# Kernel optimization log

Measured on AMD Instinct MI355X. Metric: run time of the kernel, lower is better.

Reference implementation:

```python
import jax, jax.numpy as jnp
import numpy as np

B, N, H, DQK, DV = 2, 2048, 16, 128, 128
E = H * DV
CHUNK = 64


def setup_inputs() -> dict:
    key = jax.random.key(0)
    ks = jax.random.split(key, 11)
    w = lambda k: jax.random.normal(k, (E, E), jnp.float32) * 0.02
    return {
        "x": jax.random.normal(ks[0], (B, N, E), jnp.float32),
        "prev_state": jnp.zeros((B, H, DQK, DV), jnp.float32),
        "Wq": w(ks[1]), "bq": jnp.zeros((E,), jnp.float32),
        "Wk": w(ks[2]), "bk": jnp.zeros((E,), jnp.float32),
        "Wv": w(ks[3]), "bv": jnp.zeros((E,), jnp.float32),
        "Wg": w(ks[4]), "bg": jnp.zeros((E,), jnp.float32),
        "Wo": w(ks[5]), "bo": jnp.zeros((E,), jnp.float32),
        "start_idx": 0,
    }


def _mul_i(t):
    # multiply interleaved complex pairs by i: (a, b) -> (-b, a)
    t2 = t.reshape(*t.shape[:-1], -1, 2)
    return jnp.stack((-t2[..., 1], t2[..., 0]), axis=-1).reshape(t.shape)


def reference(x, prev_state, Wq, bq, Wk, bk, Wv, bv, Wg, bg, Wo, bo, start_idx):
    b, n, e = x.shape
    h, dqk, dv, c = H, DQK, DV, CHUNK
    q = (x @ Wq.T + bq).reshape(b, n, h, dqk)
    k = (x @ Wk.T + bk).reshape(b, n, h, dqk)
    v = (x @ Wv.T + bv).reshape(b, n, h, dv)

    # xPos-style theta shift (rotary on interleaved pairs), applied along the sequence dim
    lin = jnp.linspace(0.0, 1.0, dqk // 2)
    thetas = jnp.repeat(1.0 / (10000.0 ** lin), 2).astype(x.dtype)  # (dqk,)
    idx = (start_idx + jnp.arange(n)).astype(x.dtype)
    ang = idx[:, None] * thetas[None, :]  # (n, dqk)
    sin = jnp.sin(ang)[None, :, None, :]
    cos = jnp.cos(ang)[None, :, None, :]
    q = q * cos + _mul_i(q) * sin
    k = k * cos + _mul_i(k) * sin
    k = k / jnp.sqrt(jnp.asarray(dqk, x.dtype))

    # per-head decays: 1 - 2^(-5 - h)
    gamma = 1.0 - jnp.exp2(-5.0 - jnp.arange(h, dtype=x.dtype))  # (h,)
    i = jnp.arange(c, dtype=x.dtype)
    mask = i[:, None] >= i[None, :]
    Dmat = jnp.where(mask, gamma[:, None, None] ** jnp.where(mask, i[:, None] - i[None, :], 0.0), 0.0)  # (h,c,c)
    cross_decay = gamma[:, None] ** (i[None, :] + 1.0)   # (h,c)
    kv_decay = gamma[:, None] ** (c - 1.0 - i[None, :])  # (h,c)
    chunk_decay = gamma ** c                              # (h,)

    nc = n // c
    qc = q.reshape(b, nc, c, h, dqk).transpose(1, 0, 3, 2, 4)  # (nc,b,h,c,dqk)
    kc = k.reshape(b, nc, c, h, dqk).transpose(1, 0, 3, 2, 4)
    vc = v.reshape(b, nc, c, h, dv).transpose(1, 0, 3, 2, 4)

    def step(S, qkv):
        qi, ki, vi = qkv  # (b,h,c,d)
        att = jnp.einsum('bhid,bhjd->bhij', qi, ki) * Dmat[None]
        o = jnp.einsum('bhij,bhje->bhie', att, vi)
        o = o + jnp.einsum('bhid,bhde->bhie', qi, S) * cross_decay[None, :, :, None]
        S_new = S * chunk_decay[None, :, None, None] + jnp.einsum('bhjd,bhje->bhde', ki * kv_decay[None, :, :, None], vi)
        return S_new, o

    state, outs = jax.lax.scan(step, prev_state, (qc, kc, vc))
    ret = outs.transpose(1, 0, 3, 2, 4).reshape(b, n, h, dv)

    # GroupNorm(num_groups=h, affine=False): normalize each head over dv
    mu = ret.mean(-1, keepdims=True)
    var = ((ret - mu) ** 2).mean(-1, keepdims=True)
    ret = ((ret - mu) / jnp.sqrt(var + 1e-6)).reshape(b, n, e)

    gate = jax.nn.silu(x @ Wg.T + bg)
    out = (ret * gate) @ Wo.T + bo
    return out, state
```

## Files before the change

kernel.cpp:

```cpp
#include <hip/hip_runtime.h>
#include <hip/hip_bf16.h>
#include <stdint.h>

#define B_   2
#define N_   2048
#define H_   16
#define DQK_ 128
#define DV_  128
#define E_   2048
#define CH_  64
#define NC_  32
#define M_   (B_*N_)
#define QKVG_LD 8192

using bf16x8 = __attribute__((ext_vector_type(8))) __bf16;
using f32x4  = __attribute__((ext_vector_type(4))) float;
typedef __hip_bfloat16 bf16_t;

__device__ __forceinline__ void gload_lds16(const void* g, void* l) {
  __builtin_amdgcn_global_load_lds(
      (const __attribute__((address_space(1))) void*)(uintptr_t)g,
      (__attribute__((address_space(3))) void*)(uint32_t)(uintptr_t)l,
      16, 0, 0);
}

__device__ __forceinline__ float head_log2g(int h) {
  return (float)(log2(1.0 - exp2((double)(-5 - h))));
}

__device__ __forceinline__ float bfu2f(unsigned short u) {
  unsigned int t = (unsigned int)u << 16; float f;
  __builtin_memcpy(&f, &t, 4); return f;
}
__device__ __forceinline__ unsigned short f2bfu(float f) {
  bf16_t b = __float2bfloat16(f);
  unsigned short u; __builtin_memcpy(&u, &b, 2); return u;
}

__global__ __launch_bounds__(256)
void cvt_all_kernel(const float* __restrict__ x,
                    const float* __restrict__ Wq, const float* __restrict__ Wk,
                    const float* __restrict__ Wv, const float* __restrict__ Wg,
                    const float* __restrict__ Wo,
                    const float* __restrict__ bq, const float* __restrict__ bk,
                    const float* __restrict__ bv, const float* __restrict__ bg,
                    bf16_t* __restrict__ xb, bf16_t* __restrict__ wcat,
                    bf16_t* __restrict__ wob, float* __restrict__ bcat) {
  const int NX = 2097152, NW = 1048576;
  int g = blockIdx.x * 256 + threadIdx.x;
  const float* s; bf16_t* d; int si, di;
  if (g < NX) { s = x; si = g; d = xb; di = g; }
  else if (g < NX + 4*NW) {
    int t = g - NX; int r = t / NW; si = t - r*NW;
    s = (r==0) ? Wq : (r==1) ? Wk : (r==2) ? Wv : Wg; d = wcat; di = t;
  } else if (g < NX + 5*NW) {
    si = g - NX - 4*NW; s = Wo; d = wob; di = si;
  } else {
    int j = g - (NX + 5*NW);
    int which = j >> 9, i = j & 511;
    const float* bs = (which==0) ? bq : (which==1) ? bk : (which==2) ? bv : bg;
    ((float4*)bcat)[which*512 + i] = ((const float4*)bs)[i];
    return;
  }
  float4 v = ((const float4*)s)[si];
  ushort4 p;
  p.x = f2bfu(v.x); p.y = f2bfu(v.y); p.z = f2bfu(v.z); p.w = f2bfu(v.w);
  ((ushort4*)d)[di] = p;
}

template<bool OUT_BF16, int NSUB>
__global__ __launch_bounds__(512, 2)
void gemm8_kernel(const bf16_t* __restrict__ A, const bf16_t* __restrict__ Bw,
                  const float* __restrict__ bias, void* __restrict__ Cout,
                  int K, int ldc, int tilesM) {
  extern __shared__ char smem[];
  const int nwg = gridDim.x;
  const int bid = blockIdx.x;
  const int cpx = nwg >> 3;
  const int swz = (bid & 7) * cpx + (bid >> 3);
  const int tm = swz % tilesM, tn = swz / tilesM;
  const int rowT0 = tm * 256, colT0 = tn * (64 * NSUB);
  const int tid = threadIdx.x, wave = tid >> 6, lane = tid & 63;
  const int wr = wave >> 2, wc = wave & 3;
  const int l16 = lane & 15, lhi = lane >> 4;
  const int NKT = K >> 6;

  const int sw = ((tid & 7) * 16) ^ (((tid >> 3) & 7) << 4);
  const size_t aOff = (size_t)(rowT0 + (tid >> 3)) * K + (sw >> 1);
  const size_t bOff = (size_t)(colT0 + (tid >> 3)) * K + (sw >> 1);
  const uint32_t wl = wave * 1024;

  auto stage = [&](int h) {
    const int ktp = h >> 2, r = h & 3, buf = ktp & 1;
    const int k0 = ktp << 6;
    if (r < 2) {
      const uint32_t base = 65536u + buf * (8192u*NSUB) + r * (4096u*NSUB) + wl;
#pragma unroll
      for (int L = 0; L < NSUB/2; L++)
        gload_lds16(Bw + bOff + (size_t)(r * (NSUB*32) + L * 64) * K + k0,
                    smem + base + L * 8192);
    } else {
      const int half = r - 2;
      const uint32_t base = buf * 32768u + half * 16384u + wl;
#pragma unroll
      for (int L = 0; L < 2; L++)
        gload_lds16(A + aOff + (size_t)(half * 128 + L * 64) * K + k0,
                    smem + base + L * 8192);
    }
  };

  for (int h = 0; h < 6; h++) stage(h);
  if constexpr (NSUB == 4) asm volatile("s_waitcnt vmcnt(4)" ::: "memory");
  else                     asm volatile("s_waitcnt vmcnt(2)" ::: "memory");
  __builtin_amdgcn_s_barrier();
  asm volatile("" ::: "memory");
  __builtin_amdgcn_sched_barrier(0);

  f32x4 acc[8][NSUB] = {};
  bf16x8 bfr[NSUB][2], bnx[2][2];

#pragma unroll
  for (int n = 0; n < 2; n++) {
    const int r = wc * (16*NSUB) + n * 16 + l16;
#pragma unroll
    for (int ks = 0; ks < 2; ks++) {
      const int cb = ks * 64 + lhi * 16;
      bnx[n][ks] = *(const bf16x8*)(smem + 65536u + r * 128 + (cb ^ ((r & 7) << 4)));
    }
  }

  for (int kt = 0; kt < NKT; kt++) {
    const int cur = kt & 1;
    const uint32_t aB = cur * 32768u;
    const uint32_t bB = 65536u + cur * (8192u*NSUB);
#pragma unroll
    for (int p = 0; p < 4; p++) {
      if (p == 0) {
#pragma unroll
        for (int n = 0; n < 2; n++)
#pragma unroll
          for (int ks = 0; ks < 2; ks++) bfr[n][ks] = bnx[n][ks];
        if constexpr (NSUB == 4) {
#pragma unroll
          for (int n = 2; n < 4; n++) {
            const int r = wc * (16*NSUB) + n * 16 + l16;
#pragma unroll
            for (int ks = 0; ks < 2; ks++) {
              const int cb = ks * 64 + lhi * 16;
              bfr[n][ks] = *(const bf16x8*)(smem + bB + r * 128 + (cb ^ ((r & 7) << 4)));
            }
          }
        }
      }
      bf16x8 afr[2][2];
#pragma unroll
      for (int mm = 0; mm < 2; mm++) {
        const int r = wr * 128 + p * 32 + mm * 16 + l16;
#pragma unroll
        for (int ks = 0; ks < 2; ks++) {
          const int cb = ks * 64 + lhi * 16;
          afr[mm][ks] = *(const bf16x8*)(smem + aB + r * 128 + (cb ^ ((r & 7) << 4)));
        }
      }
      const int h = 4 * kt + p + 6;
      if (h < 4 * NKT) stage(h);
      __builtin_amdgcn_s_barrier();
      asm volatile("s_waitcnt lgkmcnt(0)" ::: "memory");
      __builtin_amdgcn_sched_barrier(0);
      __builtin_amdgcn_s_setprio(1);
#pragma unroll
      for (int mm = 0; mm < 2; mm++)
#pragma unroll
        for (int n = 0; n < NSUB; n++)
#pragma unroll
          for (int ks = 0; ks < 2; ks++)
            acc[2 * p + mm][n] = __builtin_amdgcn_mfma_f32_16x16x32_bf16(
                afr[mm][ks], bfr[n][ks], acc[2 * p + mm][n], 0, 0, 0);
      __builtin_amdgcn_s_setprio(0);
      if (p == 2) {
        if constexpr (NSUB == 4) asm volatile("s_waitcnt vmcnt(6)" ::: "memory");
        else                     asm volatile("s_waitcnt vmcnt(5)" ::: "memory");
      }
      if (p == 3) {
        if (kt < NKT - 2) {
          if constexpr (NSUB == 4) asm volatile("s_waitcnt vmcnt(4)" ::: "memory");
          else                     asm volatile("s_waitcnt vmcnt(2)" ::: "memory");
        } else if (kt == NKT - 2) {
          asm volatile("s_waitcnt vmcnt(0)" ::: "memory");
        }
        if (kt + 1 < NKT) {
          const uint32_t bN = 65536u + ((kt + 1) & 1) * (8192u*NSUB);
#pragma unroll
          for (int n = 0; n < 2; n++) {
            const int r = wc * (16*NSUB) + n * 16 + l16;
#pragma unroll
            for (int ks = 0; ks < 2; ks++) {
              const int cb = ks * 64 + lhi * 16;
              bnx[n][ks] = *(const bf16x8*)(smem + bN + r * 128 + (cb ^ ((r & 7) << 4)));
            }
          }
        }
      }
      __builtin_amdgcn_s_barrier();
      asm volatile("" ::: "memory");
      __builtin_amdgcn_sched_barrier(0);
    }
  }

#pragma unroll
  for (int m = 0; m < 8; m++) {
    const int rbase = rowT0 + wr * 128 + m * 16 + lhi * 4;
#pragma unroll
    for (int n = 0; n < NSUB; n++) {
      const int col = colT0 + wc * (16*NSUB) + n * 16 + l16;
      const float bv = bias[col];
#pragma unroll
      for (int j = 0; j < 4; j++) {
        float v = acc[m][n][j] + bv;
        if (OUT_BF16) ((bf16_t*)Cout)[(size_t)(rbase + j) * ldc + col] = __float2bfloat16(v);
        else          ((float*)Cout)[(size_t)(rbase + j) * ldc + col] = v;
      }
    }
  }
}

__global__ void rotary_kernel(bf16_t* __restrict__ q, bf16_t* __restrict__ k,
                              const int* __restrict__ startp) {
  int t = blockIdx.x * 256 + threadIdx.x;
  if (t >= B_*N_*H_*16) return;
  int dg = t & 15;
  int rest = t >> 4;
  int n = (rest >> 4) & (N_ - 1);
  int h = rest & 15;
  float pos = (float)(startp[0] + n);
  size_t base = (size_t)(rest >> 4) * QKVG_LD + h * 128 + dg * 8;
  bf16x8 qv = *(const bf16x8*)(q + base);
  bf16x8 kv = *(const bf16x8*)(k + base);
  bf16x8 qo, ko;
  const float KS = 0.08838834764831843f;
#pragma unroll
  for (int p = 0; p < 4; p++) {
    int j = dg * 4 + p;
    float theta = exp2f(-13.287712379549449f * ((float)j * (1.0f/63.0f)));
    float ang = pos * theta;
    float s, c;
    sincosf(ang, &s, &c);
    float qa = (float)qv[2*p], qb = (float)qv[2*p+1];
    float ka = (float)kv[2*p], kb = (float)kv[2*p+1];
    qo[2*p]   = (__bf16)(qa*c - qb*s);
    qo[2*p+1] = (__bf16)(qb*c + qa*s);
    ko[2*p]   = (__bf16)((ka*c - kb*s) * KS);
    ko[2*p+1] = (__bf16)((kb*c + ka*s) * KS);
  }
  *(bf16x8*)(q + base) = qo;
  *(bf16x8*)(k + base) = ko;
}

__global__ __launch_bounds__(256)
void chunk_kvt_kernel(const bf16_t* __restrict__ kb, const bf16_t* __restrict__ vb,
                      bf16_t* __restrict__ kvt) {
  __shared__ alignas(16) char lds[32768];
  char* vts = lds;
  char* kts = lds + 16384;

  const int tid = threadIdx.x, wave = tid >> 6, lane = tid & 63;
  const int l16 = lane & 15, lhi = lane >> 4;
  const int blk = blockIdx.x;
  const int bh = blk >> 5, ch = blk & 31;
  const int h = bh & (H_ - 1);
  const float log2g = head_log2g(h);
  const int n0 = ch * 64;

  const size_t bhbase = (size_t)(bh >> 4) * N_ * QKVG_LD + (size_t)h * 128;

#pragma unroll
  for (int it = 0; it < 4; it++) {
    int j = it*16 + (tid >> 4);
    int e0 = (tid & 15) * 8;
    bf16x8 vv = *(const bf16x8*)(vb + bhbase + (size_t)(n0 + j)*QKVG_LD + e0);
    bf16x8 kk = *(const bf16x8*)(kb + bhbase + (size_t)(n0 + j)*QKVG_LD + e0);
    float kvd = exp2f((float)(63 - j) * log2g);
#pragma unroll
    for (int m = 0; m < 8; m++) {
      int e = e0 + m;
      *(__bf16*)(vts + e*128 + ((j*2) ^ ((e&7)<<4))) = vv[m];
      *(__bf16*)(kts + e*128 + ((j*2) ^ ((e&7)<<4))) = (__bf16)((float)kk[m] * kvd);
    }
  }
  __syncthreads();

  f32x4 acc[2][8] = {};
#pragma unroll
  for (int kk2 = 0; kk2 < 2; kk2++) {
#pragma unroll
    for (int et = 0; et < 2; et++) {
      int e = (2*wave + et)*16 + l16;
      bf16x8 vf = *(const bf16x8*)(vts + e*128 + (((kk2*32 + lhi*8)*2) ^ ((e&7)<<4)));
#pragma unroll
      for (int dt = 0; dt < 8; dt++) {
        int d = dt*16 + l16;
        bf16x8 kf = *(const bf16x8*)(kts + d*128 + (((kk2*32 + lhi*8)*2) ^ ((d&7)<<4)));
        acc[et][dt] = __builtin_amdgcn_mfma_f32_16x16x32_bf16(vf, kf, acc[et][dt], 0, 0, 0);
      }
    }
  }

  const size_t obase = (size_t)blk * 16384;
#pragma unroll
  for (int et = 0; et < 2; et++)
#pragma unroll
    for (int dt = 0; dt < 8; dt++)
#pragma unroll
      for (int j = 0; j < 4; j++) {
        int e = (2*wave + et)*16 + lhi*4 + j;
        int d = dt*16 + l16;
        kvt[obase + e*128 + d] = __float2bfloat16(acc[et][dt][j]);
      }
}

__global__ __launch_bounds__(256)
void state_scan_kernel(const bf16_t* __restrict__ kvt, const float* __restrict__ prev,
                       bf16_t* __restrict__ sbft, float* __restrict__ out_state) {
  int p = blockIdx.x * 256 + threadIdx.x;
  int bh = p >> 14;
  int ed = p & 16383;
  int e = ed >> 7, d = ed & 127;
  int h = bh & (H_ - 1);
  const float cdecay = exp2f(64.0f * head_log2g(h));

  float S = prev[(size_t)bh*16384 + d*128 + e];
  size_t boff = (size_t)bh * (NC_*16384) + ed;
  for (int ch = 0; ch < NC_; ch++) {
    sbft[boff] = __float2bfloat16(S);
    S = S * cdecay + __bfloat162float(kvt[boff]);
    boff += 16384;
  }
  out_state[(size_t)bh*16384 + d*128 + e] = S;
}

__global__ __launch_bounds__(256)
void chunk_out_kernel(const bf16_t* __restrict__ qb, const bf16_t* __restrict__ kb,
                      const bf16_t* __restrict__ vb, const bf16_t* __restrict__ gb,
                      const bf16_t* __restrict__ sbft, bf16_t* __restrict__ gated) {
  __shared__ alignas(16) char lds[32768];
  char* vts = lds;
  char* ats = lds + 16384;
  float* o_lds = (float*)lds;

  const int tid = threadIdx.x, wave = tid >> 6, lane = tid & 63;
  const int l16 = lane & 15, lhi = lane >> 4;
  const int blk = blockIdx.x;
  const int bh = blk >> 5, ch = blk & 31;
  const int h = bh & (H_ - 1);
  const int b = bh >> 4;
  const float log2g = head_log2g(h);
  const int n0 = ch * 64;

  const size_t bhbase = (size_t)b * N_ * QKVG_LD + (size_t)h * 128;
  const bf16_t* Srow = sbft + (size_t)blk * 16384;

#pragma unroll
  for (int it = 0; it < 4; it++) {
    int j = it*16 + (tid >> 4);
    int e0 = (tid & 15) * 8;
    bf16x8 vv = *(const bf16x8*)(vb + bhbase + (size_t)(n0 + j)*QKVG_LD + e0);
#pragma unroll
    for (int m = 0; m < 8; m++) {
      int e = e0 + m;
      *(__bf16*)(vts + e*128 + ((j*2) ^ ((e&7)<<4))) = vv[m];
    }
  }

  bf16x8 qf[4];
#pragma unroll
  for (int dk = 0; dk < 4; dk++)
    qf[dk] = *(const bf16x8*)(qb + bhbase + (size_t)(n0 + wave*16 + l16)*QKVG_LD + dk*32 + lhi*8);

  f32x4 aacc[4] = {};
#pragma unroll
  for (int jt = 0; jt < 4; jt++) {
#pragma unroll
    for (int dk = 0; dk < 4; dk++) {
      bf16x8 kf = *(const bf16x8*)(kb + bhbase + (size_t)(n0 + jt*16 + l16)*QKVG_LD + dk*32 + lhi*8);
      aacc[jt] = __builtin_amdgcn_mfma_f32_16x16x32_bf16(qf[dk], kf, aacc[jt], 0, 0, 0);
    }
  }
#pragma unroll
  for (int jt = 0; jt < 4; jt++)
#pragma unroll
    for (int j = 0; j < 4; j++) {
      int i = wave*16 + lhi*4 + j;
      int jc = jt*16 + l16;
      aacc[jt][j] *= (i >= jc) ? exp2f((float)(i - jc) * log2g) : 0.0f;
    }

#pragma unroll
  for (int jt = 0; jt < 4; jt++)
#pragma unroll
    for (int j = 0; j < 4; j++) {
      int i = wave*16 + lhi*4 + j;
      int jc = jt*16 + l16;
      *(__bf16*)(ats + i*128 + ((jc*2) ^ ((i&7)<<4))) = (__bf16)aacc[jt][j];
    }
  __syncthreads();

  f32x4 oacc[8] = {};
#pragma unroll
  for (int et = 0; et < 8; et++) {
#pragma unroll
    for (int dk = 0; dk < 4; dk++) {
      int e = et*16 + l16;
      bf16x8 sf = *(const bf16x8*)(Srow + e*128 + dk*32 + lhi*8);
      oacc[et] = __builtin_amdgcn_mfma_f32_16x16x32_bf16(qf[dk], sf, oacc[et], 0, 0, 0);
    }
  }
#pragma unroll
  for (int j = 0; j < 4; j++) {
    int i = wave*16 + lhi*4 + j;
    float f = exp2f((float)(i + 1) * log2g);
#pragma unroll
    for (int et = 0; et < 8; et++) oacc[et][j] *= f;
  }

#pragma unroll
  for (int kk2 = 0; kk2 < 2; kk2++) {
    int i = wave*16 + l16;
    bf16x8 af = *(const bf16x8*)(ats + i*128 + (((kk2*32 + lhi*8)*2) ^ ((i&7)<<4)));
#pragma unroll
    for (int et = 0; et < 8; et++) {
      int e = et*16 + l16;
      bf16x8 vf = *(const bf16x8*)(vts + e*128 + (((kk2*32 + lhi*8)*2) ^ ((e&7)<<4)));
      oacc[et] = __builtin_amdgcn_mfma_f32_16x16x32_bf16(af, vf, oacc[et], 0, 0, 0);
    }
  }

  __syncthreads();
#pragma unroll
  for (int et = 0; et < 8; et++)
#pragma unroll
    for (int j = 0; j < 4; j++) {
      int i = wave*16 + lhi*4 + j;
      o_lds[i*128 + et*16 + l16] = oacc[et][j];
    }
  __syncthreads();

  for (int rr = 0; rr < 16; rr++) {
    int r = wave*16 + rr;
    float2 xv = *(const float2*)&o_lds[r*128 + lane*2];
    float s = xv.x + xv.y, ss = xv.x*xv.x + xv.y*xv.y;
#pragma unroll
    for (int off = 1; off < 64; off <<= 1) {
      s  += __shfl_xor(s, off);
      ss += __shfl_xor(ss, off);
    }
    float mu  = s * (1.0f/128.0f);
    float inv = rsqrtf(ss * (1.0f/128.0f) - mu*mu + 1e-6f);
    size_t grow = (size_t)b * N_ + (n0 + r);
    unsigned int gg = *(const unsigned int*)(gb + grow*QKVG_LD + h*128 + lane*2);
    float g0 = bfu2f((unsigned short)(gg & 0xffff));
    float g1 = bfu2f((unsigned short)(gg >> 16));
    float r0 = (xv.x - mu) * inv * (g0 / (1.0f + expf(-g0)));
    float r1 = (xv.y - mu) * inv * (g1 / (1.0f + expf(-g1)));
    ushort2 o2; o2.x = f2bfu(r0); o2.y = f2bfu(r1);
    *(ushort2*)(gated + grow*2048 + h*128 + lane*2) = o2;
  }
}

extern "C" void kernel_launch(void* const* d_in, const int* in_sizes, int n_in,
                              void* d_out, int out_size, void* d_ws, size_t ws_size,
                              hipStream_t stream) {
  const float* x    = (const float*)d_in[0];
  const float* prev = (const float*)d_in[1];
  const float* Wq = (const float*)d_in[2];  const float* bq = (const float*)d_in[3];
  const float* Wk = (const float*)d_in[4];  const float* bk = (const float*)d_in[5];
  const float* Wv = (const float*)d_in[6];  const float* bv = (const float*)d_in[7];
  const float* Wg = (const float*)d_in[8];  const float* bg = (const float*)d_in[9];
  const float* Wo = (const float*)d_in[10]; const float* bo = (const float*)d_in[11];
  const int* startp = (const int*)d_in[12];

  float* out = (float*)d_out;
  float* out_state = out + (size_t)B_*N_*E_;

  char* w = (char*)d_ws;
  const size_t XN = (size_t)B_*N_*E_;
  const size_t WN = (size_t)E_*E_;
  bf16_t* xb   = (bf16_t*)w;             w += XN*2;
  bf16_t* qkvg = (bf16_t*)w;             w += (size_t)M_*QKVG_LD*2;
  bf16_t* wob  = (bf16_t*)w;             w += WN*2;
  char*   wcat_region = w;               w += 4*WN*2;
  bf16_t* wcat = (bf16_t*)wcat_region;
  bf16_t* sbft = (bf16_t*)w;             w += (size_t)B_*H_*NC_*16384*2;
  bf16_t* kvt   = (bf16_t*)wcat_region;
  float*  bcat  = (float*)sbft;

  hipFuncSetAttribute(reinterpret_cast<const void*>(gemm8_kernel<true,4>),
                      hipFuncAttributeMaxDynamicSharedMemorySize, 131072);
  hipFuncSetAttribute(reinterpret_cast<const void*>(gemm8_kernel<false,2>),
                      hipFuncAttributeMaxDynamicSharedMemorySize, 98304);

  cvt_all_kernel<<<28680, 256, 0, stream>>>(x, Wq, Wk, Wv, Wg, Wo, bq, bk, bv, bg,
                                            xb, wcat, wob, bcat);

  gemm8_kernel<true,4><<<512, 512, 131072, stream>>>(xb, wcat, bcat, (void*)qkvg,
                                                     E_, QKVG_LD, 16);

  rotary_kernel<<<(B_*N_*H_*16)/256, 256, 0, stream>>>(qkvg, qkvg + 2048, startp);

  chunk_kvt_kernel<<<B_*H_*NC_, 256, 0, stream>>>(qkvg + 2048, qkvg + 4096, kvt);
  state_scan_kernel<<<(B_*H_*16384)/256, 256, 0, stream>>>(kvt, prev, sbft, out_state);
  chunk_out_kernel<<<B_*H_*NC_, 256, 0, stream>>>(qkvg, qkvg + 2048, qkvg + 4096,
                                                  qkvg + 6144, sbft, xb );

  gemm8_kernel<false,2><<<256, 512, 98304, stream>>>(xb, wob, bo, (void*)out,
                                                     E_, E_, 16);
}
```

Before: 286.4 us.

## Fuse rotary embedding into chunk kernels and remap GEMM tile ordering

Result: slower. 306.7 us (+7.1%).

```diff
diff --git a/kernel.cpp b/kernel.cpp
--- a/kernel.cpp
+++ b/kernel.cpp
@@ -17,6 +17,9 @@
 using f32x4  = __attribute__((ext_vector_type(4))) float;
 typedef __hip_bfloat16 bf16_t;
 
+#define ROT_C 0.21091607f
+#define KS_   0.08838834764831843f
+
 __device__ __forceinline__ void gload_lds16(const void* g, void* l) {
   __builtin_amdgcn_global_load_lds(
       (const __attribute__((address_space(1))) void*)(uintptr_t)g,
@@ -35,6 +38,19 @@
 __device__ __forceinline__ unsigned short f2bfu(float f) {
   bf16_t b = __float2bfloat16(f);
   unsigned short u; __builtin_memcpy(&u, &b, 2); return u;
+}
+
+__device__ __forceinline__ void rot8(const bf16x8& v, float pos, int jp0,
+                                     float scale, float* out) {
+#pragma unroll
+  for (int p = 0; p < 4; p++) {
+    float theta = exp2f(-ROT_C * (float)(jp0 + p));
+    float ang = pos * theta, s, c;
+    sincosf(ang, &s, &c);
+    float a = (float)v[2*p], b = (float)v[2*p+1];
+    out[2*p]   = (a*c - b*s) * scale;
+    out[2*p+1] = (b*c + a*s) * scale;
+  }
 }
 
 __global__ __launch_bounds__(256)
@@ -72,13 +88,13 @@
 __global__ __launch_bounds__(512, 2)
 void gemm8_kernel(const bf16_t* __restrict__ A, const bf16_t* __restrict__ Bw,
                   const float* __restrict__ bias, void* __restrict__ Cout,
-                  int K, int ldc, int tilesM) {
+                  int K, int ldc, int tilesN) {
   extern __shared__ char smem[];
   const int nwg = gridDim.x;
   const int bid = blockIdx.x;
   const int cpx = nwg >> 3;
   const int swz = (bid & 7) * cpx + (bid >> 3);
-  const int tm = swz % tilesM, tn = swz / tilesM;
+  const int tn = swz % tilesN, tm = swz / tilesN;
   const int rowT0 = tm * 256, colT0 = tn * (64 * NSUB);
   const int tid = threadIdx.x, wave = tid >> 6, lane = tid & 63;
   const int wr = wave >> 2, wc = wave & 3;
@@ -224,41 +240,9 @@
   }
 }
 
-__global__ void rotary_kernel(bf16_t* __restrict__ q, bf16_t* __restrict__ k,
-                              const int* __restrict__ startp) {
-  int t = blockIdx.x * 256 + threadIdx.x;
-  if (t >= B_*N_*H_*16) return;
-  int dg = t & 15;
-  int rest = t >> 4;
-  int n = (rest >> 4) & (N_ - 1);
-  int h = rest & 15;
-  float pos = (float)(startp[0] + n);
-  size_t base = (size_t)(rest >> 4) * QKVG_LD + h * 128 + dg * 8;
-  bf16x8 qv = *(const bf16x8*)(q + base);
-  bf16x8 kv = *(const bf16x8*)(k + base);
-  bf16x8 qo, ko;
-  const float KS = 0.08838834764831843f;
-#pragma unroll
-  for (int p = 0; p < 4; p++) {
-    int j = dg * 4 + p;
-    float theta = exp2f(-13.287712379549449f * ((float)j * (1.0f/63.0f)));
-    float ang = pos * theta;
-    float s, c;
-    sincosf(ang, &s, &c);
-    float qa = (float)qv[2*p], qb = (float)qv[2*p+1];
-    float ka = (float)kv[2*p], kb = (float)kv[2*p+1];
-    qo[2*p]   = (__bf16)(qa*c - qb*s);
-    qo[2*p+1] = (__bf16)(qb*c + qa*s);
-    ko[2*p]   = (__bf16)((ka*c - kb*s) * KS);
-    ko[2*p+1] = (__bf16)((kb*c + ka*s) * KS);
-  }
-  *(bf16x8*)(q + base) = qo;
-  *(bf16x8*)(k + base) = ko;
-}
-
 __global__ __launch_bounds__(256)
 void chunk_kvt_kernel(const bf16_t* __restrict__ kb, const bf16_t* __restrict__ vb,
-                      bf16_t* __restrict__ kvt) {
+                      const int* __restrict__ startp, bf16_t* __restrict__ kvt) {
   __shared__ alignas(16) char lds[32768];
   char* vts = lds;
   char* kts = lds + 16384;
@@ -270,6 +254,7 @@
   const int h = bh & (H_ - 1);
   const float log2g = head_log2g(h);
   const int n0 = ch * 64;
+  const int start = startp[0];
 
   const size_t bhbase = (size_t)(bh >> 4) * N_ * QKVG_LD + (size_t)h * 128;
 
@@ -279,12 +264,14 @@
     int e0 = (tid & 15) * 8;
     bf16x8 vv = *(const bf16x8*)(vb + bhbase + (size_t)(n0 + j)*QKVG_LD + e0);
     bf16x8 kk = *(const bf16x8*)(kb + bhbase + (size_t)(n0 + j)*QKVG_LD + e0);
+    float kr[8];
+    rot8(kk, (float)(start + n0 + j), (tid & 15) * 4, KS_, kr);
     float kvd = exp2f((float)(63 - j) * log2g);
 #pragma unroll
     for (int m = 0; m < 8; m++) {
       int e = e0 + m;
       *(__bf16*)(vts + e*128 + ((j*2) ^ ((e&7)<<4))) = vv[m];
-      *(__bf16*)(kts + e*128 + ((j*2) ^ ((e&7)<<4))) = (__bf16)((float)kk[m] * kvd);
+      *(__bf16*)(kts + e*128 + ((j*2) ^ ((e&7)<<4))) = (__bf16)(kr[m] * kvd);
     }
   }
   __syncthreads();
@@ -341,7 +328,8 @@
 __global__ __launch_bounds__(256)
 void chunk_out_kernel(const bf16_t* __restrict__ qb, const bf16_t* __restrict__ kb,
                       const bf16_t* __restrict__ vb, const bf16_t* __restrict__ gb,
-                      const bf16_t* __restrict__ sbft, bf16_t* __restrict__ gated) {
+                      const bf16_t* __restrict__ sbft, const int* __restrict__ startp,
+                      bf16_t* __restrict__ gated) {
   __shared__ alignas(16) char lds[32768];
   char* vts = lds;
   char* ats = lds + 16384;
@@ -355,6 +343,7 @@
   const int b = bh >> 4;
   const float log2g = head_log2g(h);
   const int n0 = ch * 64;
+  const int start = startp[0];
 
   const size_t bhbase = (size_t)b * N_ * QKVG_LD + (size_t)h * 128;
   const bf16_t* Srow = sbft + (size_t)blk * 16384;
@@ -371,17 +360,29 @@
     }
   }
 
+  const float pos_q = (float)(start + n0 + wave*16 + l16);
   bf16x8 qf[4];
 #pragma unroll
-  for (int dk = 0; dk < 4; dk++)
-    qf[dk] = *(const bf16x8*)(qb + bhbase + (size_t)(n0 + wave*16 + l16)*QKVG_LD + dk*32 + lhi*8);
+  for (int dk = 0; dk < 4; dk++) {
+    bf16x8 qv = *(const bf16x8*)(qb + bhbase + (size_t)(n0 + wave*16 + l16)*QKVG_LD + dk*32 + lhi*8);
+    float qr[8];
+    rot8(qv, pos_q, dk*16 + lhi*4, 1.0f, qr);
+#pragma unroll
+    for (int m = 0; m < 8; m++) qf[dk][m] = (__bf16)qr[m];
+  }
 
   f32x4 aacc[4] = {};
 #pragma unroll
   for (int jt = 0; jt < 4; jt++) {
+    const float pos_k = (float)(start + n0 + jt*16 + l16);
 #pragma unroll
     for (int dk = 0; dk < 4; dk++) {
-      bf16x8 kf = *(const bf16x8*)(kb + bhbase + (size_t)(n0 + jt*16 + l16)*QKVG_LD + dk*32 + lhi*8);
+      bf16x8 kv = *(const bf16x8*)(kb + bhbase + (size_t)(n0 + jt*16 + l16)*QKVG_LD + dk*32 + lhi*8);
+      float kr[8];
+      rot8(kv, pos_k, dk*16 + lhi*4, KS_, kr);
+      bf16x8 kf;
+#pragma unroll
+      for (int m = 0; m < 8; m++) kf[m] = (__bf16)kr[m];
       aacc[jt] = __builtin_amdgcn_mfma_f32_16x16x32_bf16(qf[dk], kf, aacc[jt], 0, 0, 0);
     }
   }
@@ -502,15 +503,15 @@
                                             xb, wcat, wob, bcat);
 
   gemm8_kernel<true,4><<<512, 512, 131072, stream>>>(xb, wcat, bcat, (void*)qkvg,
-                                                     E_, QKVG_LD, 16);
-
-  rotary_kernel<<<(B_*N_*H_*16)/256, 256, 0, stream>>>(qkvg, qkvg + 2048, startp);
-
-  chunk_kvt_kernel<<<B_*H_*NC_, 256, 0, stream>>>(qkvg + 2048, qkvg + 4096, kvt);
+                                                     E_, QKVG_LD, 32 );
+
+  chunk_kvt_kernel<<<B_*H_*NC_, 256, 0, stream>>>(qkvg + 2048, qkvg + 4096,
+                                                  startp, kvt);
   state_scan_kernel<<<(B_*H_*16384)/256, 256, 0, stream>>>(kvt, prev, sbft, out_state);
   chunk_out_kernel<<<B_*H_*NC_, 256, 0, stream>>>(qkvg, qkvg + 2048, qkvg + 4096,
-                                                  qkvg + 6144, sbft, xb );
+                                                  qkvg + 6144, sbft, startp,
+                                                  xb );
 
   gemm8_kernel<false,2><<<256, 512, 98304, stream>>>(xb, wob, bo, (void*)out,
-                                                     E_, E_, 16);
-}
+                                                     E_, E_, 16 );
+}
```
